# Kernel tuning notes

Measured on AMD Instinct MI355X. Metric: run time of the kernel, lower is better.

Reference implementation:

```python
import jax, jax.numpy as jnp
import numpy as np

# B=batch, T=time, H=hidden_size, D=vocos_dim, I=intermediate_dim, L=num_layers,
# CB=codebook_size, CD=codebook_dim (factorized VQ)
B, T, H, D, I, L, CB, CD = 8, 2048, 1024, 384, 2048, 12, 8192, 8


def _ln(h, g, b, eps=1e-6):
    # torch LayerNorm over last dim (biased variance)
    m = h.mean(-1, keepdims=True)
    v = h.var(-1, keepdims=True)
    return (h - m) / jnp.sqrt(v + eps) * g + b


def _conv1d(x, w, b, groups=1):
    # x: (B, Cin, T), w: (Cout, Cin//groups, 7), same-pad k=7
    y = jax.lax.conv_general_dilated(
        x, w, window_strides=(1,), padding=[(3, 3)],
        dimension_numbers=('NCH', 'OIH', 'NCH'), feature_group_count=groups)
    return y + b[None, :, None]


def setup_inputs() -> dict:
    key = jax.random.key(0)
    ks = iter(jax.random.split(key, 32))
    def nrm(shape):
        return jax.random.normal(next(ks), shape, jnp.float32) * 0.02
    d = {}
    d['x'] = jax.random.normal(next(ks), (B, T, H), jnp.float32)
    # VocosBackbone (encoder): embed conv + LN + 12 ConvNeXt blocks + final LN
    d['enc_embed_w'] = nrm((D, H, 7)); d['enc_embed_b'] = jnp.zeros((D,), jnp.float32)
    d['enc_norm_g'] = jnp.ones((D,), jnp.float32); d['enc_norm_b'] = jnp.zeros((D,), jnp.float32)
    d['enc_dw_w'] = nrm((L, D, 1, 7)); d['enc_dw_b'] = jnp.zeros((L, D), jnp.float32)
    d['enc_ln_g'] = jnp.ones((L, D), jnp.float32); d['enc_ln_b'] = jnp.zeros((L, D), jnp.float32)
    d['enc_w1'] = nrm((L, I, D)); d['enc_b1'] = jnp.zeros((L, I), jnp.float32)
    d['enc_w2'] = nrm((L, D, I)); d['enc_b2'] = jnp.zeros((L, D), jnp.float32)
    d['enc_gamma'] = jnp.full((L, D), 1.0 / L, jnp.float32)  # layer_scale init 1/num_layers
    d['enc_fnorm_g'] = jnp.ones((D,), jnp.float32); d['enc_fnorm_b'] = jnp.zeros((D,), jnp.float32)
    # nn.Linear(vocos_dim, hidden_size)
    d['enc_out_w'] = nrm((H, D)); d['enc_out_b'] = jnp.zeros((H,), jnp.float32)
    # Factorized ResidualVQ (single quantizer): 1024 -> 8, 8192-entry codebook, 8 -> 1024
    d['vq_in_w'] = nrm((CD, H)); d['vq_in_b'] = jnp.zeros((CD,), jnp.float32)
    d['codebook'] = jax.random.normal(next(ks), (CB, CD), jnp.float32)
    d['vq_out_w'] = nrm((H, CD)); d['vq_out_b'] = jnp.zeros((H,), jnp.float32)
    return d


def _encode(x, ew, eb, ng, nb, dww, dwb, lng, lnb, w1, b1, w2, b2, gamma, fg, fb, ow, ob):
    # x: (B, T, H) -> encoder output (B, T, H)
    h = _conv1d(x.transpose(0, 2, 1), ew, eb)            # (B, D, T)
    h = _ln(h.transpose(0, 2, 1), ng, nb)                # (B, T, D)
    for i in range(L):
        res = h
        y = _conv1d(h.transpose(0, 2, 1), dww[i], dwb[i], groups=D)  # depthwise (B, D, T)
        y = _ln(y.transpose(0, 2, 1), lng[i], lnb[i])                # (B, T, D)
        y = jax.nn.gelu(y @ w1[i].T + b1[i], approximate=False)       # (B, T, I)
        y = (y @ w2[i].T + b2[i]) * gamma[i]                          # (B, T, D)
        h = res + y
    h = _ln(h, fg, fb)
    return h @ ow.T + ob                                  # (B, T, H)


def _quantize(enc, in_w, in_b, codebook, out_w, out_b):
    z_e = enc @ in_w.T + in_b                             # (B, T, CD)
    z_n = z_e / jnp.maximum(jnp.linalg.norm(z_e, axis=-1, keepdims=True), 1e-12)
    cb_n = codebook / jnp.maximum(jnp.linalg.norm(codebook, axis=-1, keepdims=True), 1e-12)
    sim = jnp.einsum('btd,nd->btn', z_n, cb_n)            # cosine sim == argmin l2 on normalized vecs
    idx = jnp.argmax(sim, axis=-1)                        # (B, T) int
    z_q = codebook[idx]                                   # (B, T, CD) unnormalized codebook entries
    z_q = z_e + jax.lax.stop_gradient(z_q - z_e)          # straight-through estimator
    quantized = z_q @ out_w.T + out_b                     # (B, T, H)
    return idx, quantized


def reference(x, enc_embed_w, enc_embed_b, enc_norm_g, enc_norm_b, enc_dw_w, enc_dw_b,
              enc_ln_g, enc_ln_b, enc_w1, enc_b1, enc_w2, enc_b2, enc_gamma,
              enc_fnorm_g, enc_fnorm_b, enc_out_w, enc_out_b,
              vq_in_w, vq_in_b, codebook, vq_out_w, vq_out_b):
    enc = _encode(x, enc_embed_w, enc_embed_b, enc_norm_g, enc_norm_b, enc_dw_w, enc_dw_b,
                  enc_ln_g, enc_ln_b, enc_w1, enc_b1, enc_w2, enc_b2, enc_gamma,
                  enc_fnorm_g, enc_fnorm_b, enc_out_w, enc_out_b)
    idx, quantized = _quantize(enc, vq_in_w, vq_in_b, codebook, vq_out_w, vq_out_b)
    # RepCodec.quantize returns (indices (B,T), quantized_out.transpose(1,2) -> (B,T,H))
    return idx, quantized
```

## Files before the change

### kernel.cpp

```cpp
#include <hip/hip_runtime.h>
#include <math.h>


typedef _Float16 h8_t __attribute__((ext_vector_type(8)));
typedef _Float16 h4_t __attribute__((ext_vector_type(4)));
typedef float f4_t __attribute__((ext_vector_type(4)));

__device__ __forceinline__ float gelu_exact(float x){
  return 0.5f * x * (1.0f + erff(x * 0.70710678118654752f));
}

__device__ __forceinline__ void split8(const float4& a, const float4& b, h8_t& hi, h8_t& lo){
  float f[8] = {a.x,a.y,a.z,a.w,b.x,b.y,b.z,b.w};
  #pragma unroll
  for (int t=0;t<8;t++){
    _Float16 hh = (_Float16)f[t];
    hi[t] = hh;
    lo[t] = (_Float16)(f[t] - (float)hh);
  }
}

__device__ __forceinline__ void split4(const float4& a, h4_t& hi, h4_t& lo){
  float f[4] = {a.x,a.y,a.z,a.w};
  #pragma unroll
  for (int t=0;t<4;t++){
    _Float16 hh = (_Float16)f[t];
    hi[t] = hh;
    lo[t] = (_Float16)(f[t] - (float)hh);
  }
}

__device__ __forceinline__ int swz(int row, int kg){
  return row*32 + ((kg ^ ((row>>1)&3))<<3);
}

__device__ __forceinline__ void xcd_remap(int& bx, int& by){
  const int gx = gridDim.x;
  const int nwg = gx * gridDim.y;
  int bid = by*gx + bx;
  if ((nwg & 7) == 0){
    bid = (bid & 7)*(nwg >> 3) + (bid >> 3);
    bx = bid % gx; by = bid / gx;
  }
}


__global__ __launch_bounds__(256) void prep_wk_split(const float* __restrict__ w,
                                                     _Float16* __restrict__ wh,
                                                     _Float16* __restrict__ wl){
  int i = blockIdx.x*256 + threadIdx.x;
  if (i >= 384*1024) return;
  int d = i >> 10, c = i & 1023;
  #pragma unroll
  for (int k=0;k<7;k++){
    float v = w[(size_t)d*(1024*7) + (size_t)c*7 + k];
    _Float16 hh = (_Float16)v;
    wh[(size_t)k*393216 + i] = hh;
    wl[(size_t)k*393216 + i] = (_Float16)(v - (float)hh);
  }
}

__global__ __launch_bounds__(256) void prep_cb(const float* __restrict__ cb, float* __restrict__ cbn){
  int e = blockIdx.x*256 + threadIdx.x;
  if (e >= 8192) return;
  float v[8], s = 0.f;
  #pragma unroll
  for (int cd=0; cd<8; ++cd){ v[cd] = cb[(size_t)e*8+cd]; s += v[cd]*v[cd]; }
  float inv = 1.0f / fmaxf(sqrtf(s), 1e-12f);
  #pragma unroll
  for (int cd=0; cd<8; ++cd) cbn[(size_t)e*8+cd] = v[cd]*inv;
}

__global__ __launch_bounds__(256) void split_pair(const float* __restrict__ a, const float* __restrict__ b,
                                                  _Float16* __restrict__ ah, _Float16* __restrict__ al,
                                                  _Float16* __restrict__ bh, _Float16* __restrict__ bl,
                                                  int n4){
  int i = blockIdx.x*256 + threadIdx.x;
  if (i >= n4) return;
  h4_t hi, lo;
  float4 va = ((const float4*)a)[i];
  split4(va, hi, lo);
  ((h4_t*)ah)[i] = hi; ((h4_t*)al)[i] = lo;
  float4 vb = ((const float4*)b)[i];
  split4(vb, hi, lo);
  ((h4_t*)bh)[i] = hi; ((h4_t*)bl)[i] = lo;
}

__global__ __launch_bounds__(256) void split_one(const float* __restrict__ a,
                                                 _Float16* __restrict__ ah, _Float16* __restrict__ al,
                                                 int n4){
  int i = blockIdx.x*256 + threadIdx.x;
  if (i >= n4) return;
  h4_t hi, lo;
  float4 va = ((const float4*)a)[i];
  split4(va, hi, lo);
  ((h4_t*)ah)[i] = hi; ((h4_t*)al)[i] = lo;
}

template<int BN, int EPI>
__global__ __launch_bounds__(256,2) void gemm_s(
    const _Float16* __restrict__ Ah, const _Float16* __restrict__ Al, int lda,
    const _Float16* __restrict__ Bh, const _Float16* __restrict__ Bl, int ldb,
    const float* __restrict__ bias, const float* __restrict__ gamma,
    float* __restrict__ C, _Float16* __restrict__ Ch, _Float16* __restrict__ Cl,
    int ldc, int K)
{
  constexpr int NF = BN/32;
  __shared__ _Float16 AsH[4096], AsL[4096];
  __shared__ _Float16 BsH[BN*32], BsL[BN*32];
  const int tid = threadIdx.x;
  int bx = blockIdx.x, by = blockIdx.y;
  xcd_remap(bx, by);
  const int m0 = by*128, n0 = bx*BN;
  const int srow = tid>>2, kgs = tid&3, koff = kgs*8;
  const _Float16* pAh = Ah + (size_t)(m0+srow)*lda + koff;
  const _Float16* pAl = Al + (size_t)(m0+srow)*lda + koff;
  const _Float16* pBh = Bh + (size_t)(n0+srow)*ldb + koff;
  const _Float16* pBl = Bl + (size_t)(n0+srow)*ldb + koff;
  const int sA0 = swz(srow, kgs), sA1 = swz(srow+64, kgs);
  const int lane = tid & 63, wid = tid >> 6;
  const int wm = (wid>>1)*64, wn = (wid&1)*(BN/2);
  const int fr = lane & 15, kg = lane >> 4;
  f4_t acc[4][NF] = {};
  h8_t rah0 = *(const h8_t*)(pAh);
  h8_t rah1 = *(const h8_t*)(pAh + (size_t)64*lda);
  h8_t ral0 = *(const h8_t*)(pAl);
  h8_t ral1 = *(const h8_t*)(pAl + (size_t)64*lda);
  h8_t rbh0 = *(const h8_t*)(pBh);
  h8_t rbl0 = *(const h8_t*)(pBl);
  h8_t rbh1, rbl1;
  if constexpr (BN == 128){
    rbh1 = *(const h8_t*)(pBh + (size_t)64*ldb);
    rbl1 = *(const h8_t*)(pBl + (size_t)64*ldb);
  }
  for (int k0 = 0; k0 < K; k0 += 32){
    __syncthreads();
    *(h8_t*)(AsH + sA0) = rah0; *(h8_t*)(AsL + sA0) = ral0;
    *(h8_t*)(AsH + sA1) = rah1; *(h8_t*)(AsL + sA1) = ral1;
    *(h8_t*)(BsH + sA0) = rbh0; *(h8_t*)(BsL + sA0) = rbl0;
    if constexpr (BN == 128){
      *(h8_t*)(BsH + sA1) = rbh1; *(h8_t*)(BsL + sA1) = rbl1;
    }
    if (k0 + 32 < K){
      const int kn = k0 + 32;
      rah0 = *(const h8_t*)(pAh + kn);
      rah1 = *(const h8_t*)(pAh + (size_t)64*lda + kn);
      ral0 = *(const h8_t*)(pAl + kn);
      ral1 = *(const h8_t*)(pAl + (size_t)64*lda + kn);
      rbh0 = *(const h8_t*)(pBh + kn);
      rbl0 = *(const h8_t*)(pBl + kn);
      if constexpr (BN == 128){
        rbh1 = *(const h8_t*)(pBh + (size_t)64*ldb + kn);
        rbl1 = *(const h8_t*)(pBl + (size_t)64*ldb + kn);
      }
    }
    __syncthreads();
    h8_t ah[4], al[4], bh[NF], bl[NF];
    #pragma unroll
    for (int m=0;m<4;m++){
      int o = swz(wm + fr + m*16, kg);
      ah[m] = *(const h8_t*)(AsH + o);
      al[m] = *(const h8_t*)(AsL + o);
    }
    #pragma unroll
    for (int n=0;n<NF;n++){
      int o = swz(wn + fr + n*16, kg);
      bh[n] = *(const h8_t*)(BsH + o);
      bl[n] = *(const h8_t*)(BsL + o);
    }
    #pragma unroll
    for (int m=0;m<4;m++)
      #pragma unroll
      for (int n=0;n<NF;n++){
        acc[m][n] = __builtin_amdgcn_mfma_f32_16x16x32_f16(al[m], bh[n], acc[m][n], 0,0,0);
        acc[m][n] = __builtin_amdgcn_mfma_f32_16x16x32_f16(ah[m], bl[n], acc[m][n], 0,0,0);
        acc[m][n] = __builtin_amdgcn_mfma_f32_16x16x32_f16(ah[m], bh[n], acc[m][n], 0,0,0);
      }
  }
  float bj[NF], gj[NF];
  #pragma unroll
  for (int n=0;n<NF;n++){
    int col = n0 + wn + n*16 + fr;
    bj[n] = bias ? bias[col] : 0.0f;
    gj[n] = (EPI==2) ? gamma[col] : 0.0f;
  }
  #pragma unroll
  for (int m=0;m<4;m++){
    #pragma unroll
    for (int r=0;r<4;r++){
      const int row = m0 + wm + m*16 + kg*4 + r;
      #pragma unroll
      for (int n=0;n<NF;n++){
        const int col = n0 + wn + n*16 + fr;
        float v = acc[m][n][r] + bj[n];
        if (EPI==0){
          C[(size_t)row*ldc + col] = v;
        } else if (EPI==1){
          v = gelu_exact(v);
          _Float16 hh = (_Float16)v;
          Ch[(size_t)row*ldc + col] = hh;
          Cl[(size_t)row*ldc + col] = (_Float16)(v - (float)hh);
        } else if (EPI==2){
          C[(size_t)row*ldc + col] += gj[n]*v;
        } else {
          _Float16 hh = (_Float16)v;
          Ch[(size_t)row*ldc + col] = hh;
          Cl[(size_t)row*ldc + col] = (_Float16)(v - (float)hh);
        }
      }
    }
  }
}

__global__ __launch_bounds__(256,2) void embed_f16(
    const float* __restrict__ x, const _Float16* __restrict__ wkh, const _Float16* __restrict__ wkl,
    const float* __restrict__ bias, float* __restrict__ C)
{
  __shared__ _Float16 AsH[4096], AsL[4096], BsH[2048], BsL[2048];
  const int tid = threadIdx.x;
  int bx = blockIdx.x, by = blockIdx.y;
  xcd_remap(bx, by);
  const int m0 = by*128, n0 = bx*64;
  const int srow = tid>>2, kgs = tid&3, koff = kgs*8;
  const int sA0 = swz(srow, kgs), sA1 = swz(srow+64, kgs);
  const int lane = tid & 63, wid = tid >> 6;
  const int wm = (wid>>1)*64, wn = (wid&1)*32;
  const int fr = lane & 15, kg = lane >> 4;
  const int r0 = m0 + srow, r1 = r0 + 64;
  const int t0 = r0 & 2047, t1 = r1 & 2047;
  f4_t acc[4][2] = {};
  for (int k=0;k<7;k++){
    const bool v0 = (unsigned)(t0 + k - 3) < 2048u;
    const bool v1 = (unsigned)(t1 + k - 3) < 2048u;
    const float* xp0 = x + (size_t)(r0 + k - 3)*1024 + koff;
    const float* xp1 = x + (size_t)(r1 + k - 3)*1024 + koff;
    const _Float16* wph = wkh + (size_t)k*393216 + (size_t)(n0+srow)*1024 + koff;
    const _Float16* wpl = wkl + (size_t)k*393216 + (size_t)(n0+srow)*1024 + koff;
    for (int k0=0;k0<1024;k0+=32){
      float4 a0a = make_float4(0,0,0,0), a0b = a0a, a1a = a0a, a1b = a0a;
      if (v0){ a0a = *(const float4*)(xp0+k0); a0b = *(const float4*)(xp0+k0+4); }
      if (v1){ a1a = *(const float4*)(xp1+k0); a1b = *(const float4*)(xp1+k0+4); }
      h8_t bvh = *(const h8_t*)(wph + k0);
      h8_t bvl = *(const h8_t*)(wpl + k0);
      __syncthreads();
      h8_t hi, lo;
      split8(a0a,a0b,hi,lo); *(h8_t*)(AsH+sA0)=hi; *(h8_t*)(AsL+sA0)=lo;
      split8(a1a,a1b,hi,lo); *(h8_t*)(AsH+sA1)=hi; *(h8_t*)(AsL+sA1)=lo;
      *(h8_t*)(BsH+sA0)=bvh; *(h8_t*)(BsL+sA0)=bvl;
      __syncthreads();
      h8_t ah[4], al[4], bh[2], bl[2];
      #pragma unroll
      for (int m=0;m<4;m++){
        int o = swz(wm + fr + m*16, kg);
        ah[m] = *(const h8_t*)(AsH + o);
        al[m] = *(const h8_t*)(AsL + o);
      }
      #pragma unroll
      for (int n=0;n<2;n++){
        int o = swz(wn + fr + n*16, kg);
        bh[n] = *(const h8_t*)(BsH + o);
        bl[n] = *(const h8_t*)(BsL + o);
      }
      #pragma unroll
      for (int m=0;m<4;m++)
        #pragma unroll
        for (int n=0;n<2;n++){
          acc[m][n] = __builtin_amdgcn_mfma_f32_16x16x32_f16(al[m], bh[n], acc[m][n], 0,0,0);
          acc[m][n] = __builtin_amdgcn_mfma_f32_16x16x32_f16(ah[m], bl[n], acc[m][n], 0,0,0);
          acc[m][n] = __builtin_amdgcn_mfma_f32_16x16x32_f16(ah[m], bh[n], acc[m][n], 0,0,0);
        }
    }
  }
  #pragma unroll
  for (int m=0;m<4;m++){
    #pragma unroll
    for (int r=0;r<4;r++){
      const int row = m0 + wm + m*16 + kg*4 + r;
      #pragma unroll
      for (int n=0;n<2;n++){
        const int col = n0 + wn + n*16 + fr;
        C[(size_t)row*384 + col] = acc[m][n][r] + bias[col];
      }
    }
  }
}

template<bool CONV, bool SPLIT>
__global__ __launch_bounds__(384) void ln_kernel(
    const float* __restrict__ in,
    const float* __restrict__ dw, const float* __restrict__ db,
    const float* __restrict__ g, const float* __restrict__ b,
    float* __restrict__ out, _Float16* __restrict__ oh, _Float16* __restrict__ ol)
{
  __shared__ float rs[6], rs2[6], stat[2];
  const int m = blockIdx.x, d = threadIdx.x;
  float v;
  if (CONV){
    const int t = m & 2047;
    float a = db[d];
    #pragma unroll
    for (int k=0;k<7;k++){
      int tt = t + k - 3;
      if ((unsigned)tt < 2048u) a = fmaf(in[(size_t)(m + k - 3)*384 + d], dw[d*7 + k], a);
    }
    v = a;
  } else {
    v = in[(size_t)m*384 + d];
  }
  float s = v, s2 = v*v;
  #pragma unroll
  for (int o=1;o<64;o<<=1){ s += __shfl_xor(s,o); s2 += __shfl_xor(s2,o); }
  const int wid = d >> 6, lane = d & 63;
  if (lane == 0){ rs[wid]=s; rs2[wid]=s2; }
  __syncthreads();
  if (d == 0){
    float S=0.f, S2=0.f;
    #pragma unroll
    for (int w=0;w<6;w++){ S+=rs[w]; S2+=rs2[w]; }
    float mean = S*(1.0f/384.0f);
    float var = fmaxf(S2*(1.0f/384.0f) - mean*mean, 0.0f);
    stat[0]=mean; stat[1]=1.0f/sqrtf(var + 1e-6f);
  }
  __syncthreads();
  float o = (v - stat[0])*stat[1]*g[d] + b[d];
  if (SPLIT){
    _Float16 hh = (_Float16)o;
    oh[(size_t)m*384 + d] = hh;
    ol[(size_t)m*384 + d] = (_Float16)(o - (float)hh);
  } else {
    out[(size_t)m*384 + d] = o;
  }
}


__global__ __launch_bounds__(256) void vq_in_kernel(
    const _Float16* __restrict__ ench, const _Float16* __restrict__ encl,
    const float* __restrict__ wi, const float* __restrict__ bi, float* __restrict__ zn)
{
  __shared__ float sw[8192];
  const int tid = threadIdx.x;
  for (int i = tid*4; i < 8192; i += 1024) *(float4*)&sw[i] = *(const float4*)&wi[i];
  __syncthreads();
  const int wid = tid >> 6, lane = tid & 63;
  const size_t m = (size_t)blockIdx.x*4 + wid;
  float acc[8] = {};
  for (int j=0;j<16;j++){
    float v = (float)ench[m*1024 + j*64 + lane] + (float)encl[m*1024 + j*64 + lane];
    #pragma unroll
    for (int cd=0;cd<8;cd++) acc[cd] = fmaf(v, sw[cd*1024 + j*64 + lane], acc[cd]);
  }
  #pragma unroll
  for (int cd=0;cd<8;cd++)
    #pragma unroll
    for (int o=1;o<64;o<<=1) acc[cd] += __shfl_xor(acc[cd], o);
  if (lane == 0){
    float z[8], s = 0.f;
    #pragma unroll
    for (int cd=0;cd<8;cd++){ z[cd] = acc[cd] + bi[cd]; s += z[cd]*z[cd]; }
    float inv = 1.0f / fmaxf(sqrtf(s), 1e-12f);
    #pragma unroll
    for (int cd=0;cd<8;cd++) zn[m*8+cd] = z[cd]*inv;
  }
}

__global__ __launch_bounds__(256) void vq_argmax(
    const float* __restrict__ zn, const float* __restrict__ cbn,
    int* __restrict__ idx_out, float* __restrict__ idx_f)
{
  __shared__ float sbest[256];
  __shared__ int   sidx[256];
  const int tid = threadIdx.x;
  const int tok = tid & 31, ch = tid >> 5;
  const size_t m = (size_t)blockIdx.x*32 + tok;
  float4 z0 = *(const float4*)&zn[m*8];
  float4 z1 = *(const float4*)&zn[m*8+4];
  float best = -1e30f; int bidx = 0;
  const float* cp = cbn + (size_t)ch*8192;
  #pragma unroll 4
  for (int e = 0; e < 1024; ++e){
    const float4 ca  = *(const float4*)&cp[e*8];
    const float4 cb4 = *(const float4*)&cp[e*8+4];
    float s = z0.x*ca.x + z0.y*ca.y + z0.z*ca.z + z0.w*ca.w
            + z1.x*cb4.x + z1.y*cb4.y + z1.z*cb4.z + z1.w*cb4.w;
    if (s > best){ best = s; bidx = ch*1024 + e; }
  }
  sbest[tid] = best; sidx[tid] = bidx;
  __syncthreads();
  if (tid < 32){
    float b = sbest[tid]; int bi = sidx[tid];
    #pragma unroll
    for (int c=1;c<8;c++){
      float ob = sbest[c*32 + tid];
      if (ob > b){ b = ob; bi = sidx[c*32 + tid]; }
    }
    idx_out[(size_t)blockIdx.x*32 + tid] = bi;
    idx_f [(size_t)blockIdx.x*32 + tid] = (float)bi;
  }
}

__global__ __launch_bounds__(256) void vq_out_kernel(
    const int* __restrict__ idx, const float* __restrict__ cb,
    const float* __restrict__ wo, const float* __restrict__ bo,
    float* __restrict__ outq)
{
  __shared__ float wT[8][1024];
  __shared__ float cbs[16][8];
  __shared__ int idxs[16];
  const int tid = threadIdx.x;
  #pragma unroll
  for (int j=0;j<4;j++){
    int hcol = j*256 + tid;
    float4 w0 = *(const float4*)&wo[(size_t)hcol*8];
    float4 w1 = *(const float4*)&wo[(size_t)hcol*8+4];
    wT[0][hcol]=w0.x; wT[1][hcol]=w0.y; wT[2][hcol]=w0.z; wT[3][hcol]=w0.w;
    wT[4][hcol]=w1.x; wT[5][hcol]=w1.y; wT[6][hcol]=w1.z; wT[7][hcol]=w1.w;
  }
  if (tid < 16) idxs[tid] = idx[blockIdx.x*16 + tid];
  __syncthreads();
  if (tid < 128){ int tk = tid>>3, cd = tid&7; cbs[tk][cd] = cb[(size_t)idxs[tk]*8 + cd]; }
  __syncthreads();
  float bb[4];
  #pragma unroll
  for (int j=0;j<4;j++) bb[j] = bo[j*256+tid];
  for (int tk=0;tk<16;tk++){
    const size_t m = (size_t)blockIdx.x*16 + tk;
    float c0=cbs[tk][0], c1=cbs[tk][1], c2=cbs[tk][2], c3=cbs[tk][3];
    float c4=cbs[tk][4], c5=cbs[tk][5], c6=cbs[tk][6], c7=cbs[tk][7];
    #pragma unroll
    for (int j=0;j<4;j++){
      int hcol = j*256 + tid;
      float v = bb[j];
      v = fmaf(c0, wT[0][hcol], v); v = fmaf(c1, wT[1][hcol], v);
      v = fmaf(c2, wT[2][hcol], v); v = fmaf(c3, wT[3][hcol], v);
      v = fmaf(c4, wT[4][hcol], v); v = fmaf(c5, wT[5][hcol], v);
      v = fmaf(c6, wT[6][hcol], v); v = fmaf(c7, wT[7][hcol], v);
      outq[m*1024 + hcol] = v;
    }
  }
}


extern "C" void kernel_launch(void* const* d_in, const int* in_sizes, int n_in,
                              void* d_out, int out_size, void* d_ws, size_t ws_size,
                              hipStream_t stream) {
  (void)in_sizes; (void)n_in; (void)out_size; (void)ws_size;
  const float* x   = (const float*)d_in[0];
  const float* eww = (const float*)d_in[1];
  const float* ewb = (const float*)d_in[2];
  const float* ng  = (const float*)d_in[3];
  const float* nb  = (const float*)d_in[4];
  const float* dww = (const float*)d_in[5];
  const float* dwb = (const float*)d_in[6];
  const float* lng = (const float*)d_in[7];
  const float* lnb = (const float*)d_in[8];
  const float* w1  = (const float*)d_in[9];
  const float* b1  = (const float*)d_in[10];
  const float* w2  = (const float*)d_in[11];
  const float* b2  = (const float*)d_in[12];
  const float* gma = (const float*)d_in[13];
  const float* fg  = (const float*)d_in[14];
  const float* fb  = (const float*)d_in[15];
  const float* ow  = (const float*)d_in[16];
  const float* ob  = (const float*)d_in[17];
  const float* viw = (const float*)d_in[18];
  const float* vib = (const float*)d_in[19];
  const float* cb  = (const float*)d_in[20];
  const float* vow = (const float*)d_in[21];
  const float* vob = (const float*)d_in[22];
  float* out = (float*)d_out;

  float* ws = (float*)d_ws;
  float* wreg = ws;
  _Float16* wkh = (_Float16*)wreg;
  _Float16* wkl = wkh + 2752512;
  _Float16* w1h = (_Float16*)wreg;
  _Float16* w1l = w1h + 786432;
  _Float16* w2h = w1h + 1572864;
  _Float16* w2l = w1h + 2359296;
  _Float16* owh = (_Float16*)wreg;
  _Float16* owl = owh + 393216;
  float* zn  = wreg + 1048576;
  float* cbn = wreg + 1179648;
  int*  idxb = (int*)(wreg + 1245184);
  float* h   = ws + 2752512;
  _Float16* ylh = (_Float16*)(ws + 9043968);
  _Float16* yll = ylh + 6291456;
  float* y1reg = ws + 15335424;
  float* yf32 = y1reg;
  _Float16* y1h = (_Float16*)y1reg;
  _Float16* y1l = y1h + 16777216;
  _Float16* ench = y1h;
  _Float16* encl = y1l;

  prep_wk_split<<<dim3(1536), dim3(256), 0, stream>>>(eww, wkh, wkl);
  embed_f16<<<dim3(6,128), dim3(256), 0, stream>>>(x, wkh, wkl, ewb, yf32);
  ln_kernel<false,false><<<dim3(16384), dim3(384), 0, stream>>>(
      yf32, nullptr, nullptr, ng, nb, h, nullptr, nullptr);

  for (int i = 0; i < 12; ++i){
    split_pair<<<dim3(768), dim3(256), 0, stream>>>(
        w1 + (size_t)i*786432, w2 + (size_t)i*786432, w1h, w1l, w2h, w2l, 196608);
    ln_kernel<true,true><<<dim3(16384), dim3(384), 0, stream>>>(
        h, dww + (size_t)i*2688, dwb + (size_t)i*384,
        lng + (size_t)i*384, lnb + (size_t)i*384, nullptr, ylh, yll);
    for (int ic = 0; ic < 2; ++ic){
      gemm_s<128,1><<<dim3(8,128), dim3(256), 0, stream>>>(
          ylh, yll, 384,
          w1h + (size_t)ic*393216, w1l + (size_t)ic*393216, 384,
          b1 + (size_t)i*2048 + (size_t)ic*1024, nullptr,
          nullptr, y1h, y1l, 1024, 384);
      gemm_s<64,2><<<dim3(6,128), dim3(256), 0, stream>>>(
          y1h, y1l, 1024,
          w2h + (size_t)ic*1024, w2l + (size_t)ic*1024, 2048,
          (ic == 0) ? (b2 + (size_t)i*384) : nullptr,
          gma + (size_t)i*384,
          h, nullptr, nullptr, 384, 1024);
    }
  }

  ln_kernel<false,true><<<dim3(16384), dim3(384), 0, stream>>>(
      h, nullptr, nullptr, fg, fb, nullptr, ylh, yll);
  split_one<<<dim3(384), dim3(256), 0, stream>>>(ow, owh, owl, 98304);
  gemm_s<128,3><<<dim3(8,128), dim3(256), 0, stream>>>(
      ylh, yll, 384, owh, owl, 384, ob, nullptr,
      nullptr, ench, encl, 1024, 384);

  prep_cb<<<dim3(32), dim3(256), 0, stream>>>(cb, cbn);
  vq_in_kernel<<<dim3(4096), dim3(256), 0, stream>>>(ench, encl, viw, vib, zn);
  vq_argmax<<<dim3(512), dim3(256), 0, stream>>>(zn, cbn, idxb, out);
  vq_out_kernel<<<dim3(1024), dim3(256), 0, stream>>>(idxb, cb, vow, vob, out + 16384);
}
```

Measured before the change: 3.752 ms.

## Add 256x128 register-prefetched GEMM, pre-split embed input, and flatten embed loop

Adds a 512-thread GEMM kernel with 256x128 tiles and register prefetch of the next K tile, used for the W1+GELU GEMMs and the output projection. This raises data reuse per block and overlaps global loads with MFMA work. The embed conv now reads input that a separate pass has already split into fp16 hi/lo, instead of splitting fp32 inside the inner loop. Its 7x32 K loop is flattened into one prefetched pipeline. The trade-off is an extra pass over x plus more workspace traffic, with heavier register and LDS use per block.

```diff
diff --git a/kernel.cpp b/kernel.cpp
--- a/kernel.cpp
+++ b/kernel.cpp
@@ -8,16 +8,6 @@
 
 __device__ __forceinline__ float gelu_exact(float x){
   return 0.5f * x * (1.0f + erff(x * 0.70710678118654752f));
-}
-
-__device__ __forceinline__ void split8(const float4& a, const float4& b, h8_t& hi, h8_t& lo){
-  float f[8] = {a.x,a.y,a.z,a.w,b.x,b.y,b.z,b.w};
-  #pragma unroll
-  for (int t=0;t<8;t++){
-    _Float16 hh = (_Float16)f[t];
-    hi[t] = hh;
-    lo[t] = (_Float16)(f[t] - (float)hh);
-  }
 }
 
 __device__ __forceinline__ void split4(const float4& a, h4_t& hi, h4_t& lo){
@@ -212,8 +202,99 @@
   }
 }
 
+template<int EPI>
+__global__ __launch_bounds__(512,2) void gemm_t(
+    const _Float16* __restrict__ Ah, const _Float16* __restrict__ Al, int lda,
+    const _Float16* __restrict__ Bh, const _Float16* __restrict__ Bl, int ldb,
+    const float* __restrict__ bias,
+    _Float16* __restrict__ Ch, _Float16* __restrict__ Cl,
+    int ldc, int K)
+{
+  __shared__ _Float16 AsH[8192], AsL[8192], BsH[4096], BsL[4096];
+  const int tid = threadIdx.x;
+  int bx = blockIdx.x, by = blockIdx.y;
+  xcd_remap(bx, by);
+  const int m0 = by*256, n0 = bx*128;
+  const int srow = tid>>2, kgs = tid&3, koff = kgs*8;
+  const _Float16* pAh = Ah + (size_t)(m0+srow)*lda + koff;
+  const _Float16* pAl = Al + (size_t)(m0+srow)*lda + koff;
+  const _Float16* pBh = Bh + (size_t)(n0+srow)*ldb + koff;
+  const _Float16* pBl = Bl + (size_t)(n0+srow)*ldb + koff;
+  const int sA0 = swz(srow, kgs), sA1 = swz(srow+128, kgs);
+  const int lane = tid & 63, wid = tid >> 6;
+  const int wm = (wid>>1)*64, wn = (wid&1)*64;
+  const int fr = lane & 15, kg = lane >> 4;
+  f4_t acc[4][4] = {};
+  h8_t rah0 = *(const h8_t*)(pAh);
+  h8_t rah1 = *(const h8_t*)(pAh + (size_t)128*lda);
+  h8_t ral0 = *(const h8_t*)(pAl);
+  h8_t ral1 = *(const h8_t*)(pAl + (size_t)128*lda);
+  h8_t rbh0 = *(const h8_t*)(pBh);
+  h8_t rbl0 = *(const h8_t*)(pBl);
+  for (int k0 = 0; k0 < K; k0 += 32){
+    __syncthreads();
+    *(h8_t*)(AsH + sA0) = rah0; *(h8_t*)(AsL + sA0) = ral0;
+    *(h8_t*)(AsH + sA1) = rah1; *(h8_t*)(AsL + sA1) = ral1;
+    *(h8_t*)(BsH + sA0) = rbh0; *(h8_t*)(BsL + sA0) = rbl0;
+    if (k0 + 32 < K){
+      const int kn = k0 + 32;
+      rah0 = *(const h8_t*)(pAh + kn);
+      rah1 = *(const h8_t*)(pAh + (size_t)128*lda + kn);
+      ral0 = *(const h8_t*)(pAl + kn);
+      ral1 = *(const h8_t*)(pAl + (size_t)128*lda + kn);
+      rbh0 = *(const h8_t*)(pBh + kn);
+      rbl0 = *(const h8_t*)(pBl + kn);
+    }
+    __syncthreads();
+    h8_t ah[4], al[4], bh[4], bl[4];
+    #pragma unroll
+    for (int m=0;m<4;m++){
+      int o = swz(wm + fr + m*16, kg);
+      ah[m] = *(const h8_t*)(AsH + o);
+      al[m] = *(const h8_t*)(AsL + o);
+    }
+    #pragma unroll
+    for (int n=0;n<4;n++){
+      int o = swz(wn + fr + n*16, kg);
+      bh[n] = *(const h8_t*)(BsH + o);
+      bl[n] = *(const h8_t*)(BsL + o);
+    }
+    #pragma unroll
+    for (int m=0;m<4;m++)
+      #pragma unroll
+      for (int n=0;n<4;n++){
+        acc[m][n] = __builtin_amdgcn_mfma_f32_16x16x32_f16(al[m], bh[n], acc[m][n], 0,0,0);
+        acc[m][n] = __builtin_amdgcn_mfma_f32_16x16x32_f16(ah[m], bl[n], acc[m][n], 0,0,0);
+        acc[m][n] = __builtin_amdgcn_mfma_f32_16x16x32_f16(ah[m], bh[n], acc[m][n], 0,0,0);
+      }
+  }
+  float bj[4];
+  #pragma unroll
+  for (int n=0;n<4;n++){
+    int col = n0 + wn + n*16 + fr;
+    bj[n] = bias ? bias[col] : 0.0f;
+  }
+  #pragma unroll
+  for (int m=0;m<4;m++){
+    #pragma unroll
+    for (int r=0;r<4;r++){
+      const int row = m0 + wm + m*16 + kg*4 + r;
+      #pragma unroll
+      for (int n=0;n<4;n++){
+        const int col = n0 + wn + n*16 + fr;
+        float v = acc[m][n][r] + bj[n];
+        if (EPI==1) v = gelu_exact(v);
+        _Float16 hh = (_Float16)v;
+        Ch[(size_t)row*ldc + col] = hh;
+        Cl[(size_t)row*ldc + col] = (_Float16)(v - (float)hh);
+      }
+    }
+  }
+}
+
 __global__ __launch_bounds__(256,2) void embed_f16(
-    const float* __restrict__ x, const _Float16* __restrict__ wkh, const _Float16* __restrict__ wkl,
+    const _Float16* __restrict__ xh, const _Float16* __restrict__ xl,
+    const _Float16* __restrict__ wkh, const _Float16* __restrict__ wkl,
     const float* __restrict__ bias, float* __restrict__ C)
 {
   __shared__ _Float16 AsH[4096], AsL[4096], BsH[2048], BsL[2048];
@@ -229,47 +310,55 @@
   const int r0 = m0 + srow, r1 = r0 + 64;
   const int t0 = r0 & 2047, t1 = r1 & 2047;
   f4_t acc[4][2] = {};
-  for (int k=0;k<7;k++){
+  const h8_t zero8 = {0,0,0,0,0,0,0,0};
+  h8_t rah0, rah1, ral0, ral1, rbh0, rbl0;
+  auto load_tile = [&](int kt, h8_t& a0, h8_t& a1, h8_t& l0, h8_t& l1, h8_t& bh, h8_t& bl){
+    const int k = kt >> 5;
+    const int k0 = (kt & 31) << 5;
     const bool v0 = (unsigned)(t0 + k - 3) < 2048u;
     const bool v1 = (unsigned)(t1 + k - 3) < 2048u;
-    const float* xp0 = x + (size_t)(r0 + k - 3)*1024 + koff;
-    const float* xp1 = x + (size_t)(r1 + k - 3)*1024 + koff;
-    const _Float16* wph = wkh + (size_t)k*393216 + (size_t)(n0+srow)*1024 + koff;
-    const _Float16* wpl = wkl + (size_t)k*393216 + (size_t)(n0+srow)*1024 + koff;
-    for (int k0=0;k0<1024;k0+=32){
-      float4 a0a = make_float4(0,0,0,0), a0b = a0a, a1a = a0a, a1b = a0a;
-      if (v0){ a0a = *(const float4*)(xp0+k0); a0b = *(const float4*)(xp0+k0+4); }
-      if (v1){ a1a = *(const float4*)(xp1+k0); a1b = *(const float4*)(xp1+k0+4); }
-      h8_t bvh = *(const h8_t*)(wph + k0);
-      h8_t bvl = *(const h8_t*)(wpl + k0);
-      __syncthreads();
-      h8_t hi, lo;
-      split8(a0a,a0b,hi,lo); *(h8_t*)(AsH+sA0)=hi; *(h8_t*)(AsL+sA0)=lo;
-      split8(a1a,a1b,hi,lo); *(h8_t*)(AsH+sA1)=hi; *(h8_t*)(AsL+sA1)=lo;
-      *(h8_t*)(BsH+sA0)=bvh; *(h8_t*)(BsL+sA0)=bvl;
-      __syncthreads();
-      h8_t ah[4], al[4], bh[2], bl[2];
-      #pragma unroll
-      for (int m=0;m<4;m++){
-        int o = swz(wm + fr + m*16, kg);
-        ah[m] = *(const h8_t*)(AsH + o);
-        al[m] = *(const h8_t*)(AsL + o);
-      }
+    a0 = zero8; a1 = zero8; l0 = zero8; l1 = zero8;
+    if (v0){
+      const size_t o = (size_t)(r0 + k - 3)*1024 + k0 + koff;
+      a0 = *(const h8_t*)(xh + o); l0 = *(const h8_t*)(xl + o);
+    }
+    if (v1){
+      const size_t o = (size_t)(r1 + k - 3)*1024 + k0 + koff;
+      a1 = *(const h8_t*)(xh + o); l1 = *(const h8_t*)(xl + o);
+    }
+    const size_t wo = (size_t)k*393216 + (size_t)(n0+srow)*1024 + k0 + koff;
+    bh = *(const h8_t*)(wkh + wo); bl = *(const h8_t*)(wkl + wo);
+  };
+  load_tile(0, rah0, rah1, ral0, ral1, rbh0, rbl0);
+  for (int kt = 0; kt < 224; ++kt){
+    __syncthreads();
+    *(h8_t*)(AsH+sA0) = rah0; *(h8_t*)(AsL+sA0) = ral0;
+    *(h8_t*)(AsH+sA1) = rah1; *(h8_t*)(AsL+sA1) = ral1;
+    *(h8_t*)(BsH+sA0) = rbh0; *(h8_t*)(BsL+sA0) = rbl0;
+    if (kt + 1 < 224)
+      load_tile(kt+1, rah0, rah1, ral0, ral1, rbh0, rbl0);
+    __syncthreads();
+    h8_t ah[4], al[4], bh[2], bl[2];
+    #pragma unroll
+    for (int m=0;m<4;m++){
+      int o = swz(wm + fr + m*16, kg);
+      ah[m] = *(const h8_t*)(AsH + o);
+      al[m] = *(const h8_t*)(AsL + o);
+    }
+    #pragma unroll
+    for (int n=0;n<2;n++){
+      int o = swz(wn + fr + n*16, kg);
+      bh[n] = *(const h8_t*)(BsH + o);
+      bl[n] = *(const h8_t*)(BsL + o);
+    }
+    #pragma unroll
+    for (int m=0;m<4;m++)
       #pragma unroll
       for (int n=0;n<2;n++){
-        int o = swz(wn + fr + n*16, kg);
-        bh[n] = *(const h8_t*)(BsH + o);
-        bl[n] = *(const h8_t*)(BsL + o);
+        acc[m][n] = __builtin_amdgcn_mfma_f32_16x16x32_f16(al[m], bh[n], acc[m][n], 0,0,0);
+        acc[m][n] = __builtin_amdgcn_mfma_f32_16x16x32_f16(ah[m], bl[n], acc[m][n], 0,0,0);
+        acc[m][n] = __builtin_amdgcn_mfma_f32_16x16x32_f16(ah[m], bh[n], acc[m][n], 0,0,0);
       }
-      #pragma unroll
-      for (int m=0;m<4;m++)
-        #pragma unroll
-        for (int n=0;n<2;n++){
-          acc[m][n] = __builtin_amdgcn_mfma_f32_16x16x32_f16(al[m], bh[n], acc[m][n], 0,0,0);
-          acc[m][n] = __builtin_amdgcn_mfma_f32_16x16x32_f16(ah[m], bl[n], acc[m][n], 0,0,0);
-          acc[m][n] = __builtin_amdgcn_mfma_f32_16x16x32_f16(ah[m], bh[n], acc[m][n], 0,0,0);
-        }
-    }
   }
   #pragma unroll
   for (int m=0;m<4;m++){
@@ -483,17 +572,21 @@
   float* cbn = wreg + 1179648;
   int*  idxb = (int*)(wreg + 1245184);
   float* h   = ws + 2752512;
-  _Float16* ylh = (_Float16*)(ws + 9043968);
+  float* ylreg = ws + 9043968;
+  float* yf32 = ylreg;
+  _Float16* ylh = (_Float16*)ylreg;
   _Float16* yll = ylh + 6291456;
   float* y1reg = ws + 15335424;
-  float* yf32 = y1reg;
+  _Float16* xh  = (_Float16*)y1reg;
+  _Float16* xl  = xh + 16777216;
   _Float16* y1h = (_Float16*)y1reg;
   _Float16* y1l = y1h + 16777216;
   _Float16* ench = y1h;
   _Float16* encl = y1l;
 
   prep_wk_split<<<dim3(1536), dim3(256), 0, stream>>>(eww, wkh, wkl);
-  embed_f16<<<dim3(6,128), dim3(256), 0, stream>>>(x, wkh, wkl, ewb, yf32);
+  split_one<<<dim3(16384), dim3(256), 0, stream>>>(x, xh, xl, 4194304);
+  embed_f16<<<dim3(6,128), dim3(256), 0, stream>>>(xh, xl, wkh, wkl, ewb, yf32);
   ln_kernel<false,false><<<dim3(16384), dim3(384), 0, stream>>>(
       yf32, nullptr, nullptr, ng, nb, h, nullptr, nullptr);
 
@@ -504,11 +597,11 @@
         h, dww + (size_t)i*2688, dwb + (size_t)i*384,
         lng + (size_t)i*384, lnb + (size_t)i*384, nullptr, ylh, yll);
     for (int ic = 0; ic < 2; ++ic){
-      gemm_s<128,1><<<dim3(8,128), dim3(256), 0, stream>>>(
+      gemm_t<1><<<dim3(8,64), dim3(512), 0, stream>>>(
           ylh, yll, 384,
           w1h + (size_t)ic*393216, w1l + (size_t)ic*393216, 384,
-          b1 + (size_t)i*2048 + (size_t)ic*1024, nullptr,
-          nullptr, y1h, y1l, 1024, 384);
+          b1 + (size_t)i*2048 + (size_t)ic*1024,
+          y1h, y1l, 1024, 384);
       gemm_s<64,2><<<dim3(6,128), dim3(256), 0, stream>>>(
           y1h, y1l, 1024,
           w2h + (size_t)ic*1024, w2l + (size_t)ic*1024, 2048,
@@ -521,9 +614,8 @@
   ln_kernel<false,true><<<dim3(16384), dim3(384), 0, stream>>>(
       h, nullptr, nullptr, fg, fb, nullptr, ylh, yll);
   split_one<<<dim3(384), dim3(256), 0, stream>>>(ow, owh, owl, 98304);
-  gemm_s<128,3><<<dim3(8,128), dim3(256), 0, stream>>>(
-      ylh, yll, 384, owh, owl, 384, ob, nullptr,
-      nullptr, ench, encl, 1024, 384);
+  gemm_t<3><<<dim3(8,64), dim3(512), 0, stream>>>(
+      ylh, yll, 384, owh, owl, 384, ob, ench, encl, 1024, 384);
 
   prep_cb<<<dim3(32), dim3(256), 0, stream>>>(cb, cbn);
   vq_in_kernel<<<dim3(4096), dim3(256), 0, stream>>>(ench, encl, viw, vib, zn);
```

After: 3.732 ms. About the same (-0.5%).
